# Optimization experiments

Hardware: AMD Instinct MI355X
Metric: run time of the kernel (lower is better)

## Reference

```python
import jax, jax.numpy as jnp
import numpy as np

B, S, T = 256, 2048, 64


def setup_inputs() -> dict:
    key = jax.random.key(0)
    k1, k2, k3, k4, k5 = jax.random.split(key, 5)
    emissions = jax.random.normal(k1, (B, S, T), dtype=jnp.float32)
    tags = jax.random.randint(k2, (B, S), 0, T)
    mask = jnp.ones((B, S), dtype=jnp.int32)
    start_transitions = jax.random.uniform(k3, (T,), minval=-1.0, maxval=1.0, dtype=jnp.float32)
    end_transitions = jax.random.uniform(k4, (T,), minval=-1.0, maxval=1.0, dtype=jnp.float32)
    transitions = jax.random.uniform(k5, (T, T), minval=-1.0, maxval=1.0, dtype=jnp.float32)
    return {
        'emissions': emissions,
        'start_transitions': start_transitions,
        'end_transitions': end_transitions,
        'transitions': transitions,
        'tags': tags,
        'mask': mask,
    }


def _crf_nll(emissions, start_transitions, end_transitions, transitions, tags, mask):
    # batch_first=True -> convert to time-major like the torch code
    em = jnp.swapaxes(emissions, 0, 1)            # (S, B, T)
    tg = tags.T                                   # (S, B)
    mk = mask.T.astype(emissions.dtype)           # (S, B)
    barange = jnp.arange(em.shape[1])

    # ---- numerator: score of the gold tag path ----
    score0 = start_transitions[tg[0]] + em[0, barange, tg[0]]  # (B,)

    def num_step(score, inp):
        em_i, tg_prev, tg_i, m_i = inp
        score = score + (transitions[tg_prev, tg_i] + em_i[barange, tg_i]) * m_i
        return score, None

    numerator, _ = jax.lax.scan(num_step, score0, (em[1:], tg[:-1], tg[1:], mk[1:]))
    seq_ends = mk.sum(axis=0).astype(jnp.int32) - 1            # (B,)
    last_tags = tg[seq_ends, barange]
    numerator = numerator + end_transitions[last_tags]

    # ---- denominator: log partition via forward algorithm (log-sum-exp semiring) ----
    alpha0 = start_transitions + em[0]                          # (B, T)

    def den_step(alpha, inp):
        em_i, m_i = inp
        # (B, T_prev, T_next) broadcast-add, reduce over T_prev
        nxt = jax.nn.logsumexp(alpha[:, :, None] + transitions[None, :, :] + em_i[:, None, :], axis=1)
        alpha = jnp.where(m_i[:, None] > 0, nxt, alpha)
        return alpha, None

    alpha, _ = jax.lax.scan(den_step, alpha0, (em[1:], mk[1:]))
    denominator = jax.nn.logsumexp(alpha + end_transitions, axis=1)  # (B,)

    return -(numerator - denominator).mean()


def reference(emissions, start_transitions, end_transitions, transitions, tags, mask):
    return _crf_nll(emissions, start_transitions, end_transitions, transitions, tags, mask)
```

## Files before the change

### kernel.cpp

```cpp
#include <hip/hip_runtime.h>

#define BB 256
#define SS 2048
#define TT 64
#define KC 64
#define LC 32
#define WARM 48
#define NSTEP (WARM + LC)
#define DEN_WAVES (BB * 4)
#define NSLOT 128
#define SLOT_STRIDE 32
#define LN2 0.69314718055994531f
#define LOG2E 1.4426950408889634f

typedef __fp16 half2v __attribute__((ext_vector_type(2)));
typedef __fp16 half8v __attribute__((ext_vector_type(8)));
typedef float float4v __attribute__((ext_vector_type(4)));

__device__ __forceinline__ float4v mfma16(half8v a, half8v b, float4v c) {
  return __builtin_amdgcn_mfma_f32_16x16x32_f16(a, b, c, 0, 0, 0);
}

__global__ __launch_bounds__(64) void crf_kernel(
    const float* __restrict__ em, const float* __restrict__ startT,
    const float* __restrict__ endT, const float* __restrict__ trans,
    const int* __restrict__ tags, const int* __restrict__ mask,
    float* __restrict__ acc, int slotmask) {
  const int lane = threadIdx.x;

  if (blockIdx.x >= DEN_WAVES) {
    const int bb = blockIdx.x - DEN_WAVES;
    const int* tg = tags + bb * SS;
    const int* mp = mask + bb * SS;
    const float* emb = em + (size_t)bb * SS * TT;
    float part = 0.f;
    int cnt = 0;
#pragma unroll 4
    for (int k = 0; k < SS / 64; ++k) {
      int i = k * 64 + lane;
      int m = mp[i];
      cnt += m;
      if (i >= 1 && m) {
        int t1 = tg[i], t0 = tg[i - 1];
        part += trans[t0 * TT + t1] + emb[(size_t)i * TT + t1];
      }
    }
#pragma unroll
    for (int o = 32; o > 0; o >>= 1) {
      part += __shfl_xor(part, o, 64);
      cnt += __shfl_xor(cnt, o, 64);
    }
    if (lane == 0) {
      int t0 = tg[0];
      float num = part + startT[t0] + emb[t0] + endT[tg[cnt - 1]];
      atomicAdd(acc + (size_t)(blockIdx.x & slotmask) * SLOT_STRIDE,
                -num * (1.0f / BB));
    }
    return;
  }

  const int w = blockIdx.x;
  const int L = (w & 7) * (DEN_WAVES / 8) + (w >> 3);
  const int bb = L >> 2;
  const int quarter = L & 3;
  const int s = lane & 15;
  const int g = lane >> 4;
  const int c = quarter * 16 + s;
  const float* emB = em + (size_t)bb * SS * TT;
  const size_t rowb = (size_t)bb * SS;

  half8v A[4][2];
#pragma unroll
  for (int mt = 0; mt < 4; ++mt)
#pragma unroll
    for (int kt = 0; kt < 2; ++kt) {
      half8v f;
#pragma unroll
      for (int e = 0; e < 8; e += 2) {
        int k0 = 32 * kt + 16 * (e >> 2) + 4 * g + (e & 3);
        int m = 16 * mt + s;
        float v0 = __expf(trans[k0 * TT + m]) * 0.03125f;
        float v1 = __expf(trans[(k0 + 1) * TT + m]) * 0.03125f;
        half2v p = __builtin_amdgcn_cvt_pkrtz(v0, v1);
        f[e] = p[0];
        f[e + 1] = p[1];
      }
      A[mt][kt] = f;
    }

  half8v B0, B1;
#pragma unroll
  for (int e = 0; e < 8; ++e) {
    B0[e] = (__fp16)0.015625f;
    B1[e] = (__fp16)0.015625f;
  }
  float q0cur = 0.015625f;
  int esum = 0, nsteps = 0;
  float sS = 0.f, gamma = 0.f;
  float4v tf0, tf1, tf2, tf3;

  const int base = c * LC - WARM + 1;

  float4v buf[4][4];

  auto PF = [&](int slot, int idx) {
    int p = base + idx;
    p = p < 0 ? 0 : (p > SS - 1 ? SS - 1 : p);
    const float* r = emB + (size_t)p * TT + 4 * g;
#pragma unroll
    for (int mt = 0; mt < 4; ++mt) buf[slot][mt] = *(const float4v*)(r + 16 * mt);
  };
  auto CORE = [&](const float4v (&x)[4]) {
    const float4v z = {0.f, 0.f, 0.f, 0.f};
    tf0 = mfma16(A[0][0], B0, z);
    tf0 = mfma16(A[0][1], B1, tf0);
    float rv = tf0[0] * x[0][0];
    float v = __shfl(rv, s, 64);
    tf1 = mfma16(A[1][0], B0, z);
    tf1 = mfma16(A[1][1], B1, tf1);
    tf2 = mfma16(A[2][0], B0, z);
    tf2 = mfma16(A[2][1], B1, tf2);
    tf3 = mfma16(A[3][0], B0, z);
    tf3 = mfma16(A[3][1], B1, tf3);
    tf0 *= x[0]; tf1 *= x[1]; tf2 *= x[2]; tf3 *= x[3];
    int eb = __builtin_bit_cast(int, v) & 0x7f800000;
    float sc = __builtin_bit_cast(float, 0x7C000000 - eb);
    esum += eb >> 23;
    nsteps += 1;
    q0cur = v * sc;
    tf0 *= sc; tf1 *= sc; tf2 *= sc; tf3 *= sc;
    half2v p;
    p = __builtin_amdgcn_cvt_pkrtz(tf0[0], tf0[1]); B0[0] = p[0]; B0[1] = p[1];
    p = __builtin_amdgcn_cvt_pkrtz(tf0[2], tf0[3]); B0[2] = p[0]; B0[3] = p[1];
    p = __builtin_amdgcn_cvt_pkrtz(tf1[0], tf1[1]); B0[4] = p[0]; B0[5] = p[1];
    p = __builtin_amdgcn_cvt_pkrtz(tf1[2], tf1[3]); B0[6] = p[0]; B0[7] = p[1];
    p = __builtin_amdgcn_cvt_pkrtz(tf2[0], tf2[1]); B1[0] = p[0]; B1[1] = p[1];
    p = __builtin_amdgcn_cvt_pkrtz(tf2[2], tf2[3]); B1[2] = p[0]; B1[3] = p[1];
    p = __builtin_amdgcn_cvt_pkrtz(tf3[0], tf3[1]); B1[4] = p[0]; B1[5] = p[1];
    p = __builtin_amdgcn_cvt_pkrtz(tf3[2], tf3[3]); B1[6] = p[0]; B1[7] = p[1];
  };
  auto STEP = [&](int slot, int pfIdx, bool doPf) {
    float4v x[4];
#pragma unroll
    for (int mt = 0; mt < 4; ++mt)
#pragma unroll
      for (int e = 0; e < 4; ++e) x[mt][e] = __expf(buf[slot][mt][e]);
    if (doPf) PF(slot, pfIdx);
    CORE(x);
  };

#pragma unroll
  for (int k = 0; k < 4; ++k) PF(k, k);

  for (int idx = 0; idx < WARM; idx += 4) {
#pragma unroll
    for (int k = 0; k < 4; ++k) STEP(k, idx + k + 4, true);
  }

  sS = __log2f(q0cur) + (float)(6 + esum - 116 * nsteps);
  if (c == 0) {
    float aref = startT[0] + emB[0];
    gamma = aref * LOG2E;
    sS = 0.f;
    esum = 0;
    nsteps = 0;
    q0cur = 0.015625f;
#pragma unroll
    for (int e = 0; e < 8; ++e) {
      int t0i = 16 * (e >> 2) + 4 * g + (e & 3);
      B0[e] = (__fp16)(__expf(startT[t0i] + emB[t0i] - aref) * 0.015625f);
      B1[e] = (__fp16)(__expf(startT[t0i + 32] + emB[t0i + 32] - aref) *
                       0.015625f);
    }
  }

  for (int idx = WARM; idx < NSTEP - 4; idx += 4) {
#pragma unroll
    for (int k = 0; k < 4; ++k) STEP(k, idx + k + 4, true);
  }
  STEP(0, 0, false);
  STEP(1, 0, false);
  STEP(2, 0, false);
  {
    half8v oB0 = B0, oB1 = B1;
    float4v o0 = tf0, o1 = tf1, o2 = tf2, o3 = tf3;
    int oes = esum, on = nsteps;
    float oq = q0cur;
    STEP(3, 0, false);
    int p = base + (NSTEP - 1);
    int pc = p > SS - 1 ? SS - 1 : p;
    bool act = (p >= 1) && (p <= SS - 1) && (mask[rowb + pc] != 0);
    if (!act) {
      B0 = oB0; B1 = oB1; esum = oes; nsteps = on; q0cur = oq;
      tf0 = o0; tf1 = o1; tf2 = o2; tf3 = o3;
    }
  }

  float eS = __log2f(q0cur) + (float)(6 + esum - 116 * nsteps) + gamma;
  float contrib = LN2 * (eS - sS);

  {
    float q0l = __log2f(q0cur);
    float4v ar0, ar1, ar2, ar3;
    float mx = -1e30f;
#pragma unroll
    for (int r = 0; r < 4; ++r) {
      ar0[r] = LN2 * (__log2f(tf0[r]) - q0l) + endT[4 * g + r];
      ar1[r] = LN2 * (__log2f(tf1[r]) - q0l) + endT[16 + 4 * g + r];
      ar2[r] = LN2 * (__log2f(tf2[r]) - q0l) + endT[32 + 4 * g + r];
      ar3[r] = LN2 * (__log2f(tf3[r]) - q0l) + endT[48 + 4 * g + r];
      mx = fmaxf(mx, fmaxf(fmaxf(ar0[r], ar1[r]), fmaxf(ar2[r], ar3[r])));
    }
    mx = fmaxf(mx, __shfl_xor(mx, 16, 64));
    mx = fmaxf(mx, __shfl_xor(mx, 32, 64));
    float ex = 0.f;
#pragma unroll
    for (int r = 0; r < 4; ++r)
      ex += __expf(ar0[r] - mx) + __expf(ar1[r] - mx) + __expf(ar2[r] - mx) +
            __expf(ar3[r] - mx);
    ex += __shfl_xor(ex, 16, 64);
    ex += __shfl_xor(ex, 32, 64);
    if (c == KC - 1) contrib += mx + __logf(ex);
  }

  float val = (g == 0) ? contrib : 0.f;
#pragma unroll
  for (int o = 32; o > 0; o >>= 1) val += __shfl_xor(val, o, 64);
  if (lane == 0)
    atomicAdd(acc + (size_t)(blockIdx.x & slotmask) * SLOT_STRIDE,
              val * (1.0f / BB));
}

__global__ __launch_bounds__(64) void reduce_kernel(const float* __restrict__ ws,
                                                    float* __restrict__ out) {
  float v = ws[(size_t)threadIdx.x * SLOT_STRIDE] +
            ws[(size_t)(threadIdx.x + 64) * SLOT_STRIDE];
#pragma unroll
  for (int o = 32; o > 0; o >>= 1) v += __shfl_xor(v, o, 64);
  if (threadIdx.x == 0) *out = v;
}

extern "C" void kernel_launch(void* const* d_in, const int* in_sizes, int n_in,
                              void* d_out, int out_size, void* d_ws, size_t ws_size,
                              hipStream_t stream) {
  const float* em = (const float*)d_in[0];
  const float* startT = (const float*)d_in[1];
  const float* endT = (const float*)d_in[2];
  const float* trans = (const float*)d_in[3];
  const int* tags = (const int*)d_in[4];
  const int* mask = (const int*)d_in[5];
  float* out = (float*)d_out;

  const size_t need = (size_t)NSLOT * SLOT_STRIDE * sizeof(float);
  if (d_ws && ws_size >= need) {
    (void)hipMemsetAsync(d_ws, 0, need, stream);
    crf_kernel<<<DEN_WAVES + BB, 64, 0, stream>>>(em, startT, endT, trans, tags,
                                                  mask, (float*)d_ws, NSLOT - 1);
    reduce_kernel<<<1, 64, 0, stream>>>((const float*)d_ws, out);
  } else {
    (void)hipMemsetAsync(out, 0, sizeof(float), stream);
    crf_kernel<<<DEN_WAVES + BB, 64, 0, stream>>>(em, startT, endT, trans, tags,
                                                  mask, out, 0);
  }
}
```

Measured before the change: 252.8 us.

## Split sequence into more, shorter chunks and move rescale off the MFMA critical path

Doubles the number of time chunks per sequence (KC 128, LC 16), so each batch row uses eight waves and each wave runs a shorter serial forward recursion. It also adds a launch-bounds occupancy hint. The per-step exponent rescale now uses the value shuffled out in the previous step and is applied to the emissions before the MFMAs, so the shuffle no longer sits between the MFMA results and the next step. The cost is more total warm-up work, since the 48 warm-up steps are repeated for twice as many chunks, plus a one-step lag in the normalisation, which could affect fp16 range.

```diff
diff --git a/kernel.cpp b/kernel.cpp
--- a/kernel.cpp
+++ b/kernel.cpp
@@ -3,11 +3,11 @@
 #define BB 256
 #define SS 2048
 #define TT 64
-#define KC 64
-#define LC 32
+#define KC 128
+#define LC 16
 #define WARM 48
 #define NSTEP (WARM + LC)
-#define DEN_WAVES (BB * 4)
+#define DEN_WAVES (BB * 8)
 #define NSLOT 128
 #define SLOT_STRIDE 32
 #define LN2 0.69314718055994531f
@@ -21,7 +21,7 @@
   return __builtin_amdgcn_mfma_f32_16x16x32_f16(a, b, c, 0, 0, 0);
 }
 
-__global__ __launch_bounds__(64) void crf_kernel(
+__global__ __launch_bounds__(64, 2) void crf_kernel(
     const float* __restrict__ em, const float* __restrict__ startT,
     const float* __restrict__ endT, const float* __restrict__ trans,
     const int* __restrict__ tags, const int* __restrict__ mask,
@@ -61,11 +61,10 @@
 
   const int w = blockIdx.x;
   const int L = (w & 7) * (DEN_WAVES / 8) + (w >> 3);
-  const int bb = L >> 2;
-  const int quarter = L & 3;
+  const int bb = L >> 3;
   const int s = lane & 15;
   const int g = lane >> 4;
-  const int c = quarter * 16 + s;
+  const int c = (L & 7) * 16 + s;
   const float* emB = em + (size_t)bb * SS * TT;
   const size_t rowb = (size_t)bb * SS;
 
@@ -94,7 +93,7 @@
     B0[e] = (__fp16)0.015625f;
     B1[e] = (__fp16)0.015625f;
   }
-  float q0cur = 0.015625f;
+  float v_ready = 0.015625f;
   int esum = 0, nsteps = 0;
   float sS = 0.f, gamma = 0.f;
   float4v tf0, tf1, tf2, tf3;
@@ -111,24 +110,22 @@
     for (int mt = 0; mt < 4; ++mt) buf[slot][mt] = *(const float4v*)(r + 16 * mt);
   };
   auto CORE = [&](const float4v (&x)[4]) {
+    int eb = __builtin_bit_cast(int, v_ready) & 0x7f800000;
+    float sc = __builtin_bit_cast(float, 0x7C000000 - eb);
+    esum += eb >> 23;
+    nsteps += 1;
+    float4v xs0 = x[0] * sc, xs1 = x[1] * sc, xs2 = x[2] * sc, xs3 = x[3] * sc;
     const float4v z = {0.f, 0.f, 0.f, 0.f};
     tf0 = mfma16(A[0][0], B0, z);
     tf0 = mfma16(A[0][1], B1, tf0);
-    float rv = tf0[0] * x[0][0];
-    float v = __shfl(rv, s, 64);
     tf1 = mfma16(A[1][0], B0, z);
     tf1 = mfma16(A[1][1], B1, tf1);
     tf2 = mfma16(A[2][0], B0, z);
     tf2 = mfma16(A[2][1], B1, tf2);
     tf3 = mfma16(A[3][0], B0, z);
     tf3 = mfma16(A[3][1], B1, tf3);
-    tf0 *= x[0]; tf1 *= x[1]; tf2 *= x[2]; tf3 *= x[3];
-    int eb = __builtin_bit_cast(int, v) & 0x7f800000;
-    float sc = __builtin_bit_cast(float, 0x7C000000 - eb);
-    esum += eb >> 23;
-    nsteps += 1;
-    q0cur = v * sc;
-    tf0 *= sc; tf1 *= sc; tf2 *= sc; tf3 *= sc;
+    tf0 *= xs0; tf1 *= xs1; tf2 *= xs2; tf3 *= xs3;
+    v_ready = __shfl(tf0[0], s, 64);
     half2v p;
     p = __builtin_amdgcn_cvt_pkrtz(tf0[0], tf0[1]); B0[0] = p[0]; B0[1] = p[1];
     p = __builtin_amdgcn_cvt_pkrtz(tf0[2], tf0[3]); B0[2] = p[0]; B0[3] = p[1];
@@ -157,20 +154,23 @@
     for (int k = 0; k < 4; ++k) STEP(k, idx + k + 4, true);
   }
 
-  sS = __log2f(q0cur) + (float)(6 + esum - 116 * nsteps);
-  if (c == 0) {
-    float aref = startT[0] + emB[0];
-    gamma = aref * LOG2E;
-    sS = 0.f;
-    esum = 0;
-    nsteps = 0;
-    q0cur = 0.015625f;
-#pragma unroll
-    for (int e = 0; e < 8; ++e) {
-      int t0i = 16 * (e >> 2) + 4 * g + (e & 3);
-      B0[e] = (__fp16)(__expf(startT[t0i] + emB[t0i] - aref) * 0.015625f);
-      B1[e] = (__fp16)(__expf(startT[t0i + 32] + emB[t0i + 32] - aref) *
-                       0.015625f);
+  {
+    float q0b = v_ready;
+    sS = __log2f(q0b) + (float)(6 + esum - 116 * nsteps);
+    if (c == 0) {
+      float aref = startT[0] + emB[0];
+      gamma = aref * LOG2E;
+      sS = 0.f;
+      esum = 0;
+      nsteps = 0;
+      v_ready = 0.015625f;
+#pragma unroll
+      for (int e = 0; e < 8; ++e) {
+        int t0i = 16 * (e >> 2) + 4 * g + (e & 3);
+        B0[e] = (__fp16)(__expf(startT[t0i] + emB[t0i] - aref) * 0.015625f);
+        B1[e] = (__fp16)(__expf(startT[t0i + 32] + emB[t0i + 32] - aref) *
+                         0.015625f);
+      }
     }
   }
 
@@ -181,26 +181,28 @@
   STEP(0, 0, false);
   STEP(1, 0, false);
   STEP(2, 0, false);
+  float qf;
   {
     half8v oB0 = B0, oB1 = B1;
     float4v o0 = tf0, o1 = tf1, o2 = tf2, o3 = tf3;
     int oes = esum, on = nsteps;
-    float oq = q0cur;
+    float ov = v_ready;
     STEP(3, 0, false);
     int p = base + (NSTEP - 1);
     int pc = p > SS - 1 ? SS - 1 : p;
     bool act = (p >= 1) && (p <= SS - 1) && (mask[rowb + pc] != 0);
+    qf = act ? v_ready : ov;
     if (!act) {
-      B0 = oB0; B1 = oB1; esum = oes; nsteps = on; q0cur = oq;
+      B0 = oB0; B1 = oB1; esum = oes; nsteps = on;
       tf0 = o0; tf1 = o1; tf2 = o2; tf3 = o3;
     }
   }
 
-  float eS = __log2f(q0cur) + (float)(6 + esum - 116 * nsteps) + gamma;
+  float eS = __log2f(qf) + (float)(6 + esum - 116 * nsteps) + gamma;
   float contrib = LN2 * (eS - sS);
 
   {
-    float q0l = __log2f(q0cur);
+    float q0l = __log2f(qf);
     float4v ar0, ar1, ar2, ar3;
     float mx = -1e30f;
 #pragma unroll
```

Result: slower. 283.1 us (+12.0%).
